# Optimization experiments

Hardware: AMD Instinct MI355X
Metric: run time of the kernel (lower is better)

Reference implementation:

```python
import jax, jax.numpy as jnp
import numpy as np
import math

B, N, D = 64, 512, 1024
SHELL_DIM, RFF_DIM, ORDER = 64, 32, 4
CHARGE_COUPLING, SHELL_COUPLING = 1.0, 0.5
DIST_COUPLING, DIST_SCALE = 0.3, 10.0
COMBINED_DIM = 64


def setup_inputs() -> dict:
    key = jax.random.key(0)
    ks = jax.random.split(key, 12)
    s = 0.02
    inp = {
        "x": jax.random.normal(ks[0], (B, N, D), dtype=jnp.float32),
        "W_charge": jax.random.normal(ks[1], (1, D), dtype=jnp.float32) * s,
        "b_charge": jnp.zeros((1,), dtype=jnp.float32),
        "W_shell": jax.random.normal(ks[2], (SHELL_DIM, D), dtype=jnp.float32) * s,
        "b_shell": jnp.zeros((SHELL_DIM,), dtype=jnp.float32),
        # RFF params (learnable=True in source): omega ~ N(0,1)*sqrt(coupling), bias ~ U(0, 2pi)
        "omega": jax.random.normal(ks[3], (RFF_DIM, SHELL_DIM), dtype=jnp.float32) * math.sqrt(SHELL_COUPLING),
        "rff_bias": jax.random.uniform(ks[4], (RFF_DIM,), dtype=jnp.float32) * (2.0 * math.pi),
        "W_combine": jax.random.normal(ks[5], (COMBINED_DIM, (ORDER + 1) * 2 * RFF_DIM), dtype=jnp.float32) * s,
        "W_v": jax.random.normal(ks[6], (D, D), dtype=jnp.float32) * s,
        "b_v": jnp.zeros((D,), dtype=jnp.float32),
        "W_out": jax.random.normal(ks[7], (D, D), dtype=jnp.float32) * s,
        "b_out": jnp.zeros((D,), dtype=jnp.float32),
        "log_temp": jnp.zeros((), dtype=jnp.float32),
    }
    return inp


def _forward(x, W_charge, b_charge, W_shell, b_shell, omega, rff_bias,
             W_combine, W_v, b_v, W_out, b_out, log_temp):
    b, n, d = x.shape
    # charge: (B,N) in [-1,1]
    q = jnp.tanh(x @ W_charge.T + b_charge)[..., 0]
    # polynomial charge features: sqrt(|(-k)^n/n!| + 1e-10) * q^n, n=0..ORDER
    coeffs = jnp.asarray([(-CHARGE_COUPLING) ** m / math.factorial(m) for m in range(ORDER + 1)], dtype=x.dtype)
    mags = jnp.sqrt(jnp.abs(coeffs) + 1e-10)  # (5,)
    phi_c = mags * q[..., None] ** jnp.arange(ORDER + 1)  # (B,N,5)
    # shell: normalized linear projection
    shell = x @ W_shell.T + b_shell
    shell = shell / jnp.maximum(jnp.linalg.norm(shell, axis=-1, keepdims=True), 1e-12)
    # random Fourier features
    proj = shell @ omega.T + rff_bias  # (B,N,RFF)
    rff_scale = math.sqrt(2.0 / (2 * RFF_DIM)) * math.sqrt(math.exp(-SHELL_COUPLING))
    phi_s = jnp.concatenate([jnp.cos(proj), jnp.sin(proj)], axis=-1) * rff_scale  # (B,N,64)
    # tensor product -> combine projection (no bias)
    tp = (phi_c[..., :, None] * phi_s[..., None, :]).reshape(b, n, -1)  # (B,N,5*64)
    phi = tp @ W_combine.T  # (B,N,64)
    # Toeplitz distance weighting exp(-coupling*|i-j|/scale)
    idx = jnp.arange(n)
    T = jnp.exp(-DIST_COUPLING * jnp.abs(idx[:, None] - idx[None, :]).astype(x.dtype) / DIST_SCALE)
    temp = jax.nn.softplus(log_temp) + 0.1
    logits = jnp.einsum('bnd,bmd->bnm', phi, phi) * T / temp
    # causal mask (allow j <= i)
    causal = idx[:, None] >= idx[None, :]
    logits = jnp.where(causal, logits, -jnp.inf)
    attn = jax.nn.softmax(logits, axis=-1)
    V = x @ W_v.T + b_v
    out = jnp.einsum('bnm,bmd->bnd', attn, V)
    return out @ W_out.T + b_out


def reference(x, W_charge, b_charge, W_shell, b_shell, omega, rff_bias,
              W_combine, W_v, b_v, W_out, b_out, log_temp):
    return _forward(x, W_charge, b_charge, W_shell, b_shell, omega, rff_bias,
                    W_combine, W_v, b_v, W_out, b_out, log_temp)
```

## Files before the change

### kernel.cpp

```cpp
#include <hip/hip_runtime.h>
#include <hip/hip_bf16.h>
#include <math.h>


using u16 = unsigned short;
typedef short short8 __attribute__((ext_vector_type(8)));
typedef float f32x4 __attribute__((ext_vector_type(4)));

__device__ __forceinline__ u16 f2bf(float f) {
  unsigned u = __float_as_uint(f);
  return (u16)((u + 0x7fffu + ((u >> 16) & 1u)) >> 16);
}

__device__ __forceinline__ void gload16(const u16* g, u16* l) {
  __builtin_amdgcn_global_load_lds(
      (const __attribute__((address_space(1))) unsigned int*)(g),
      (__attribute__((address_space(3))) unsigned int*)(l),
      16, 0, 0);
}

__global__ __launch_bounds__(256) void convert_x_kernel(const float* __restrict__ in,
                                                        u16* __restrict__ out, int n4) {
  int idx = blockIdx.x * 256 + threadIdx.x;
  int stride = gridDim.x * 256;
  for (int i = idx; i < n4; i += stride) {
    float4 v = reinterpret_cast<const float4*>(in)[i];
    ushort4 o;
    o.x = f2bf(v.x); o.y = f2bf(v.y); o.z = f2bf(v.z); o.w = f2bf(v.w);
    reinterpret_cast<ushort4*>(out)[i] = o;
  }
}

__global__ __launch_bounds__(256) void prep_weights_kernel(
    const float* __restrict__ Wv, const float* __restrict__ Wo,
    const float* __restrict__ Wsh, const float* __restrict__ Wch,
    const float* __restrict__ Wcb,
    u16* __restrict__ wvb, u16* __restrict__ wob,
    u16* __restrict__ wcat, u16* __restrict__ wcbb) {
  int i = blockIdx.x * 256 + threadIdx.x;
  if (i < 1048576) { wvb[i] = f2bf(Wv[i]); return; }
  i -= 1048576;
  if (i < 1048576) { wob[i] = f2bf(Wo[i]); return; }
  i -= 1048576;
  if (i < 131072) {
    int row = i >> 10, e = i & 1023;
    float v = (row < 64) ? Wsh[i] : ((row == 64) ? Wch[e] : 0.0f);
    wcat[i] = f2bf(v);
    return;
  }
  i -= 131072;
  if (i < 40960) {
    int row = i / 320;
    wcbb[i] = f2bf(row < 64 ? Wcb[i] : 0.0f);
  }
}

template<int OUT_MODE>
__global__ __launch_bounds__(256) void gemm_bt(
    const u16* __restrict__ A, const u16* __restrict__ Bt,
    const float* __restrict__ bias, void* __restrict__ Cv,
    int M, int N, int K, int lda, int ldb, int ldc,
    long long sA, long long sB, long long sC) {
  (void)M; (void)N;
  __shared__ u16 lA[128 * 32];
  __shared__ u16 lB[128 * 32];
  const int t = threadIdx.x;
  const int lane = t & 63;
  const int w = t >> 6;
  const u16* Ag = A + (size_t)blockIdx.z * sA;
  const u16* Bg = Bt + (size_t)blockIdx.z * sB;

  int gx = gridDim.x, gy = gridDim.y;
  int bid = blockIdx.y * gx + blockIdx.x;
  int nwg = gx * gy;
  if ((nwg & 7) == 0) {
    int cpx = nwg >> 3;
    bid = (bid & 7) * cpx + (bid >> 3);
  }
  const int m0 = (bid / gx) * 128;
  const int n0 = (bid % gx) * 128;

  const int wm = (w >> 1) * 64;
  const int wn = (w & 1) * 64;
  const int rl = lane & 15;
  const int kl = (lane >> 4) * 8;

  const int rs = w * 32 + (lane >> 2);
  const int cs = (lane & 3) * 8;
  u16* ldsA = &lA[w * 1024];
  u16* ldsB = &lB[w * 1024];

  f32x4 acc[4][4] = {};

  for (int k0 = 0; k0 < K; k0 += 32) {
    const u16* ga = Ag + (size_t)(m0 + rs) * lda + k0 + cs;
    const u16* gb = Bg + (size_t)(n0 + rs) * ldb + k0 + cs;
    gload16(ga,                      ldsA);
    gload16(ga + (size_t)16 * lda,   ldsA + 512);
    gload16(gb,                      ldsB);
    gload16(gb + (size_t)16 * ldb,   ldsB + 512);
    __syncthreads();
    short8 af[4], bfr[4];
    #pragma unroll
    for (int mi = 0; mi < 4; ++mi)
      af[mi] = *reinterpret_cast<const short8*>(&lA[(wm + mi * 16 + rl) * 32 + kl]);
    #pragma unroll
    for (int ni = 0; ni < 4; ++ni)
      bfr[ni] = *reinterpret_cast<const short8*>(&lB[(wn + ni * 16 + rl) * 32 + kl]);
    #pragma unroll
    for (int mi = 0; mi < 4; ++mi) {
      #pragma unroll
      for (int ni = 0; ni < 4; ++ni)
        acc[mi][ni] = __builtin_amdgcn_mfma_f32_16x16x32_bf16(af[mi], bfr[ni], acc[mi][ni], 0, 0, 0);
    }
    __syncthreads();
  }

  const int cm = (lane >> 4) * 4;
  #pragma unroll
  for (int mi = 0; mi < 4; ++mi) {
    #pragma unroll
    for (int ni = 0; ni < 4; ++ni) {
      const int gm = m0 + wm + mi * 16 + cm;
      const int gn = n0 + wn + ni * 16 + rl;
      const float bsv = bias ? bias[gn] : 0.0f;
      if (OUT_MODE == 0) {
        float* C = (float*)Cv + (size_t)blockIdx.z * sC;
        #pragma unroll
        for (int r = 0; r < 4; ++r)
          C[(size_t)(gm + r) * ldc + gn] = acc[mi][ni][r] + bsv;
      } else if (OUT_MODE == 1) {
        u16* C = (u16*)Cv + (size_t)blockIdx.z * sC;
        #pragma unroll
        for (int r = 0; r < 4; ++r)
          C[(size_t)(gm + r) * ldc + gn] = f2bf(acc[mi][ni][r] + bsv);
      } else {
        u16* C = (u16*)Cv + (size_t)blockIdx.z * sC;
        ushort4 pk;
        pk.x = f2bf(acc[mi][ni][0] + bsv);
        pk.y = f2bf(acc[mi][ni][1] + bsv);
        pk.z = f2bf(acc[mi][ni][2] + bsv);
        pk.w = f2bf(acc[mi][ni][3] + bsv);
        *reinterpret_cast<ushort4*>(&C[(size_t)gn * ldc + gm]) = pk;
      }
    }
  }
}

__global__ __launch_bounds__(256) void features_kernel(
    const float* __restrict__ SC, const float* __restrict__ b_shell,
    const float* __restrict__ b_charge, const float* __restrict__ omega,
    const float* __restrict__ rff_bias, u16* __restrict__ tp) {
  __shared__ __align__(16) float sm[4][64];
  const int lane = threadIdx.x & 63;
  const int w = threadIdx.x >> 6;
  const int row = blockIdx.x * 4 + w;
  const float* sc = SC + (size_t)row * 128;
  float s = sc[lane] + b_shell[lane];
  float ss = s * s;
  #pragma unroll
  for (int off = 32; off > 0; off >>= 1) ss += __shfl_xor(ss, off);
  float shell = s / fmaxf(sqrtf(ss), 1e-12f);
  sm[w][lane] = shell;
  const float q = tanhf(sc[64] + b_charge[0]);
  __syncthreads();
  const int r = lane & 31;
  float p = rff_bias[r];
  const float4* om = reinterpret_cast<const float4*>(omega + r * 64);
  const float4* sv = reinterpret_cast<const float4*>(sm[w]);
  #pragma unroll
  for (int d = 0; d < 16; ++d) {
    float4 o4 = om[d], s4 = sv[d];
    p += o4.x * s4.x + o4.y * s4.y + o4.z * s4.z + o4.w * s4.w;
  }
  const float RFFS = 0.13767388f;
  float phis = (lane < 32) ? cosf(p) * RFFS : sinf(p) * RFFS;
  float q2 = q * q;
  float pc[5];
  pc[0] = 1.0f;
  pc[1] = q;
  pc[2] = 0.70710678f * q2;
  pc[3] = 0.40824829f * q2 * q;
  pc[4] = 0.20412415f * q2 * q2;
  u16* o = tp + (size_t)row * 320 + lane;
  #pragma unroll
  for (int m = 0; m < 5; ++m) o[m * 64] = f2bf(pc[m] * phis);
}

__global__ __launch_bounds__(256) void softmax_kernel(
    const float* __restrict__ logits, const float* __restrict__ log_temp,
    u16* __restrict__ attn) {
  __shared__ float rb[8];
  const int rowid = blockIdx.x;
  const int i = rowid & 511;
  const float* L = logits + (size_t)rowid * 512;
  u16* Ar = attn + (size_t)rowid * 512;
  const int t = threadIdx.x, lane = t & 63, w = t >> 6;
  const float invt = 1.0f / (log1pf(expf(log_temp[0])) + 0.1f);
  const int j0 = t, j1 = t + 256;
  float z0 = (j0 <= i) ? L[j0] * expf(-0.03f * (float)(i - j0)) * invt : -INFINITY;
  float z1 = (j1 <= i) ? L[j1] * expf(-0.03f * (float)(i - j1)) * invt : -INFINITY;
  float m = fmaxf(z0, z1);
  #pragma unroll
  for (int off = 32; off > 0; off >>= 1) m = fmaxf(m, __shfl_xor(m, off));
  if (lane == 0) rb[w] = m;
  __syncthreads();
  m = fmaxf(fmaxf(rb[0], rb[1]), fmaxf(rb[2], rb[3]));
  float e0 = expf(z0 - m);
  float e1 = expf(z1 - m);
  float sum = e0 + e1;
  #pragma unroll
  for (int off = 32; off > 0; off >>= 1) sum += __shfl_xor(sum, off);
  if (lane == 0) rb[4 + w] = sum;
  __syncthreads();
  const float inv = 1.0f / (rb[4] + rb[5] + rb[6] + rb[7]);
  Ar[j0] = f2bf(e0 * inv);
  Ar[j1] = f2bf(e1 * inv);
}

extern "C" void kernel_launch(void* const* d_in, const int* in_sizes, int n_in,
                              void* d_out, int out_size, void* d_ws, size_t ws_size,
                              hipStream_t stream) {
  (void)in_sizes; (void)n_in; (void)out_size; (void)ws_size;
  const float* x     = (const float*)d_in[0];
  const float* Wch   = (const float*)d_in[1];
  const float* bch   = (const float*)d_in[2];
  const float* Wsh   = (const float*)d_in[3];
  const float* bsh   = (const float*)d_in[4];
  const float* omega = (const float*)d_in[5];
  const float* rffb  = (const float*)d_in[6];
  const float* Wcb   = (const float*)d_in[7];
  const float* Wv    = (const float*)d_in[8];
  const float* bv    = (const float*)d_in[9];
  const float* Wo    = (const float*)d_in[10];
  const float* bo    = (const float*)d_in[11];
  const float* lt    = (const float*)d_in[12];
  float* out = (float*)d_out;
  char* ws = (char*)d_ws;

  u16*   xb   = (u16*)(ws + 0);
  u16*   vt   = (u16*)(ws + 67108864);
  float* sc   = (float*)(ws + 67108864);
  u16*   attn = (u16*)(ws + 134217728);
  u16*   tp   = (u16*)(ws + 134217728);
  u16*   phi  = (u16*)(ws + 167772160);
  u16*   wvb  = (u16*)(ws + 176160768);
  u16*   wob  = (u16*)(ws + 178257920);
  u16*   wcat = (u16*)(ws + 180355072);
  u16*   wcbb = (u16*)(ws + 180617216);
  float* logits = out;
  u16*   out2 = xb;

  convert_x_kernel<<<8192, 256, 0, stream>>>(x, xb, 33554432 / 4);
  prep_weights_kernel<<<8864, 256, 0, stream>>>(Wv, Wo, Wsh, Wch, Wcb, wvb, wob, wcat, wcbb);
  gemm_bt<0><<<dim3(1, 256, 1), 256, 0, stream>>>(xb, wcat, nullptr, sc,
      32768, 128, 1024, 1024, 1024, 128, 0, 0, 0);
  features_kernel<<<8192, 256, 0, stream>>>(sc, bsh, bch, omega, rffb, tp);
  gemm_bt<1><<<dim3(1, 256, 1), 256, 0, stream>>>(tp, wcbb, nullptr, phi,
      32768, 128, 320, 320, 320, 128, 0, 0, 0);
  gemm_bt<0><<<dim3(4, 4, 64), 256, 0, stream>>>(phi, phi, nullptr, logits,
      512, 512, 64, 128, 128, 512, 65536, 65536, 262144);
  softmax_kernel<<<32768, 256, 0, stream>>>(logits, lt, attn);
  gemm_bt<2><<<dim3(8, 256, 1), 256, 0, stream>>>(xb, wvb, bv, vt,
      32768, 1024, 1024, 1024, 1024, 32768, 0, 0, 0);
  gemm_bt<1><<<dim3(8, 4, 64), 256, 0, stream>>>(attn, vt, nullptr, out2,
      512, 1024, 512, 512, 32768, 1024, 262144, 512, 524288);
  gemm_bt<0><<<dim3(8, 256, 1), 256, 0, stream>>>(out2, wob, bo, out,
      32768, 1024, 1024, 1024, 1024, 1024, 0, 0, 0);
}
```

Measured before the change: 684.9 us.

## Add 256x256 double-buffered swizzled-LDS GEMM for the three large matmuls

Adds a new gemm256 kernel that uses 256x256 output tiles with 8 waves, a K-step of 64, and double-buffered LDS filled by direct global-to-LDS loads. LDS is XOR-swizzled to avoid bank conflicts, and s_setprio is raised around the MFMA bursts. The V projection, attn@V and output projection now use it in place of the 128x128 single-buffered kernel. The goal is more data reuse per tile and overlap of the next tile's loads with compute. The cost is 128KB of LDS per block and heavy register use, which limits occupancy.

```diff
diff --git a/kernel.cpp b/kernel.cpp
--- a/kernel.cpp
+++ b/kernel.cpp
@@ -12,11 +12,16 @@
   return (u16)((u + 0x7fffu + ((u >> 16) & 1u)) >> 16);
 }
 
-__device__ __forceinline__ void gload16(const u16* g, u16* l) {
+__device__ __forceinline__ void gload16(const u16* g, const u16* l) {
   __builtin_amdgcn_global_load_lds(
       (const __attribute__((address_space(1))) unsigned int*)(g),
       (__attribute__((address_space(3))) unsigned int*)(l),
       16, 0, 0);
+}
+
+__device__ __forceinline__ short8 ldsrd(const u16* base, int row, int b) {
+  int byte = row * 128 + (b ^ ((row & 7) << 4));
+  return *reinterpret_cast<const short8*>(reinterpret_cast<const char*>(base) + byte);
 }
 
 __global__ __launch_bounds__(256) void convert_x_kernel(const float* __restrict__ in,
@@ -56,6 +61,122 @@
 }
 
 template<int OUT_MODE>
+__global__ __launch_bounds__(512, 2) void gemm256(
+    const u16* __restrict__ A, const u16* __restrict__ Bt,
+    const float* __restrict__ bias, void* __restrict__ Cv,
+    int M, int N, int K, int lda, int ldb, int ldc,
+    long long sA, long long sB, long long sC) {
+  (void)M; (void)N;
+  __shared__ u16 lds[65536];
+  const int t = threadIdx.x;
+  const int lane = t & 63;
+  const int w = t >> 6;
+  const u16* Ag = A + (size_t)blockIdx.z * sA;
+  const u16* Bg = Bt + (size_t)blockIdx.z * sB;
+
+  int gx = gridDim.x, gy = gridDim.y;
+  int bid = blockIdx.y * gx + blockIdx.x;
+  int nwg = gx * gy;
+  if ((nwg & 7) == 0) { int cpx = nwg >> 3; bid = (bid & 7) * cpx + (bid >> 3); }
+  const int m0 = (bid / gx) * 256;
+  const int n0 = (bid % gx) * 256;
+
+  const int wm = w >> 2;
+  const int wn = w & 3;
+  const int rl = lane & 15;
+  const int kq = lane >> 4;
+
+  const int srow = w * 8 + (lane >> 3);
+  const int scol = 8 * ((lane & 7) ^ ((lane >> 3) & 7));
+  const u16* aS = Ag + (size_t)(m0 + srow) * lda + scol;
+  const u16* bS = Bg + (size_t)(n0 + srow) * ldb + scol;
+
+  const int NT = K >> 6;
+
+  #pragma unroll
+  for (int g = 0; g < 4; ++g) {
+    gload16(aS + (size_t)(g * 64) * lda, lds + w * 512 + g * 4096);
+    gload16(bS + (size_t)(g * 64) * ldb, lds + 16384 + w * 512 + g * 4096);
+  }
+
+  f32x4 acc[8][4] = {};
+
+  for (int tt = 0; tt < NT; ++tt) {
+    const int c = tt & 1, nc = c ^ 1;
+    const u16* At  = lds + c * 32768;
+    const u16* Btl = At + 16384;
+    const u16* dA  = lds + nc * 32768 + w * 512;
+    const u16* dB  = dA + 16384;
+    const int kn = (tt + 1 < NT ? tt + 1 : 0) << 6;
+
+    __builtin_amdgcn_s_barrier();
+    #pragma unroll
+    for (int g = 0; g < 4; ++g) {
+      gload16(aS + (size_t)(g * 64) * lda + kn, dA + g * 4096);
+      gload16(bS + (size_t)(g * 64) * ldb + kn, dB + g * 4096);
+    }
+    asm volatile("s_waitcnt vmcnt(8)" ::: "memory");
+    __builtin_amdgcn_s_barrier();
+    __builtin_amdgcn_sched_barrier(0);
+
+    short8 bq[4][2];
+    #pragma unroll
+    for (int p = 0; p < 4; ++p) {
+      if (p == 0) {
+        #pragma unroll
+        for (int ni = 0; ni < 4; ++ni)
+          #pragma unroll
+          for (int ks = 0; ks < 2; ++ks)
+            bq[ni][ks] = ldsrd(Btl, wn * 64 + ni * 16 + rl, ks * 64 + kq * 16);
+      }
+      short8 a0k0 = ldsrd(At, wm * 128 + (2 * p + 0) * 16 + rl, 0 + kq * 16);
+      short8 a0k1 = ldsrd(At, wm * 128 + (2 * p + 0) * 16 + rl, 64 + kq * 16);
+      short8 a1k0 = ldsrd(At, wm * 128 + (2 * p + 1) * 16 + rl, 0 + kq * 16);
+      short8 a1k1 = ldsrd(At, wm * 128 + (2 * p + 1) * 16 + rl, 64 + kq * 16);
+      __builtin_amdgcn_s_setprio(1);
+      #pragma unroll
+      for (int ni = 0; ni < 4; ++ni) {
+        acc[2 * p][ni]     = __builtin_amdgcn_mfma_f32_16x16x32_bf16(a0k0, bq[ni][0], acc[2 * p][ni], 0, 0, 0);
+        acc[2 * p][ni]     = __builtin_amdgcn_mfma_f32_16x16x32_bf16(a0k1, bq[ni][1], acc[2 * p][ni], 0, 0, 0);
+        acc[2 * p + 1][ni] = __builtin_amdgcn_mfma_f32_16x16x32_bf16(a1k0, bq[ni][0], acc[2 * p + 1][ni], 0, 0, 0);
+        acc[2 * p + 1][ni] = __builtin_amdgcn_mfma_f32_16x16x32_bf16(a1k1, bq[ni][1], acc[2 * p + 1][ni], 0, 0, 0);
+      }
+      __builtin_amdgcn_s_setprio(0);
+    }
+  }
+
+  const int cm = (lane >> 4) * 4;
+  #pragma unroll
+  for (int mi = 0; mi < 8; ++mi) {
+    #pragma unroll
+    for (int ni = 0; ni < 4; ++ni) {
+      const int gm = m0 + wm * 128 + mi * 16 + cm;
+      const int gn = n0 + wn * 64 + ni * 16 + rl;
+      const float bsv = bias ? bias[gn] : 0.0f;
+      if (OUT_MODE == 0) {
+        float* C = (float*)Cv + (size_t)blockIdx.z * sC;
+        #pragma unroll
+        for (int r = 0; r < 4; ++r)
+          C[(size_t)(gm + r) * ldc + gn] = acc[mi][ni][r] + bsv;
+      } else if (OUT_MODE == 1) {
+        u16* C = (u16*)Cv + (size_t)blockIdx.z * sC;
+        #pragma unroll
+        for (int r = 0; r < 4; ++r)
+          C[(size_t)(gm + r) * ldc + gn] = f2bf(acc[mi][ni][r] + bsv);
+      } else {
+        u16* C = (u16*)Cv + (size_t)blockIdx.z * sC;
+        ushort4 pk;
+        pk.x = f2bf(acc[mi][ni][0] + bsv);
+        pk.y = f2bf(acc[mi][ni][1] + bsv);
+        pk.z = f2bf(acc[mi][ni][2] + bsv);
+        pk.w = f2bf(acc[mi][ni][3] + bsv);
+        *reinterpret_cast<ushort4*>(&C[(size_t)gn * ldc + gm]) = pk;
+      }
+    }
+  }
+}
+
+template<int OUT_MODE>
 __global__ __launch_bounds__(256) void gemm_bt(
     const u16* __restrict__ A, const u16* __restrict__ Bt,
     const float* __restrict__ bias, void* __restrict__ Cv,
@@ -73,10 +194,7 @@
   int gx = gridDim.x, gy = gridDim.y;
   int bid = blockIdx.y * gx + blockIdx.x;
   int nwg = gx * gy;
-  if ((nwg & 7) == 0) {
-    int cpx = nwg >> 3;
-    bid = (bid & 7) * cpx + (bid >> 3);
-  }
+  if ((nwg & 7) == 0) { int cpx = nwg >> 3; bid = (bid & 7) * cpx + (bid >> 3); }
   const int m0 = (bid / gx) * 128;
   const int n0 = (bid % gx) * 128;
 
@@ -84,7 +202,6 @@
   const int wn = (w & 1) * 64;
   const int rl = lane & 15;
   const int kl = (lane >> 4) * 8;
-
   const int rs = w * 32 + (lane >> 2);
   const int cs = (lane & 3) * 8;
   u16* ldsA = &lA[w * 1024];
@@ -95,10 +212,10 @@
   for (int k0 = 0; k0 < K; k0 += 32) {
     const u16* ga = Ag + (size_t)(m0 + rs) * lda + k0 + cs;
     const u16* gb = Bg + (size_t)(n0 + rs) * ldb + k0 + cs;
-    gload16(ga,                      ldsA);
-    gload16(ga + (size_t)16 * lda,   ldsA + 512);
-    gload16(gb,                      ldsB);
-    gload16(gb + (size_t)16 * ldb,   ldsB + 512);
+    gload16(ga,                    ldsA);
+    gload16(ga + (size_t)16 * lda, ldsA + 512);
+    gload16(gb,                    ldsB);
+    gload16(gb + (size_t)16 * ldb, ldsB + 512);
     __syncthreads();
     short8 af[4], bfr[4];
     #pragma unroll
@@ -261,10 +378,10 @@
   gemm_bt<0><<<dim3(4, 4, 64), 256, 0, stream>>>(phi, phi, nullptr, logits,
       512, 512, 64, 128, 128, 512, 65536, 65536, 262144);
   softmax_kernel<<<32768, 256, 0, stream>>>(logits, lt, attn);
-  gemm_bt<2><<<dim3(8, 256, 1), 256, 0, stream>>>(xb, wvb, bv, vt,
+  gemm256<2><<<dim3(4, 128, 1), 512, 0, stream>>>(xb, wvb, bv, vt,
       32768, 1024, 1024, 1024, 1024, 32768, 0, 0, 0);
-  gemm_bt<1><<<dim3(8, 4, 64), 256, 0, stream>>>(attn, vt, nullptr, out2,
+  gemm256<1><<<dim3(4, 2, 64), 512, 0, stream>>>(attn, vt, nullptr, out2,
       512, 1024, 512, 512, 32768, 1024, 262144, 512, 524288);
-  gemm_bt<0><<<dim3(8, 256, 1), 256, 0, stream>>>(out2, wob, bo, out,
+  gemm256<0><<<dim3(4, 128, 1), 512, 0, stream>>>(out2, wob, bo, out,
       32768, 1024, 1024, 1024, 1024, 1024, 0, 0, 0);
 }
```

Measured after the change: 635.2 us. 7.3% less time.
